# Kernel optimization log

Measured on AMD Instinct MI355X. Metric: run time of the kernel, lower is better.

Reference implementation:

```python
import jax, jax.numpy as jnp
import numpy as np

E = 8        # n_routed_experts
K = 2        # n_experts_per_token
H = 1024     # d_hidden
D = 512      # d_expert
NSH = 2      # n_shared_experts -> shared expert width = D*NSH


def setup_inputs() -> dict:
    key = jax.random.key(0)
    ks = jax.random.split(key, 8)
    s = 0.02
    x = jax.random.normal(ks[0], (4, 2048, H), jnp.float32)
    W_router = (jax.random.normal(ks[1], (H, E), jnp.float32) * s)
    Wg = (jax.random.normal(ks[2], (E, H, D), jnp.float32) * s)   # per-expert gate proj
    Wu = (jax.random.normal(ks[3], (E, H, D), jnp.float32) * s)   # per-expert up proj
    Wd = (jax.random.normal(ks[4], (E, D, H), jnp.float32) * s)   # per-expert down proj
    Ds = D * NSH
    Wsg = (jax.random.normal(ks[5], (H, Ds), jnp.float32) * s)
    Wsu = (jax.random.normal(ks[6], (H, Ds), jnp.float32) * s)
    Wsd = (jax.random.normal(ks[7], (Ds, H), jnp.float32) * s)
    return {"x": x, "W_router": W_router, "Wg": Wg, "Wu": Wu, "Wd": Wd,
            "Wsg": Wsg, "Wsu": Wsu, "Wsd": Wsd}


def reference(x, W_router, Wg, Wu, Wd, Wsg, Wsu, Wsd):
    B, S, Hd = x.shape
    T = B * S
    xf = x.reshape(T, Hd)

    # shared expert (SwiGLU)
    shared = (jax.nn.silu(xf @ Wsg) * (xf @ Wsu)) @ Wsd          # [T, H]

    # gating: softmax -> top-k -> renormalize
    logits = xf @ W_router                                        # [T, E]
    probs = jax.nn.softmax(logits, axis=-1)
    topk_scores, topk_idx = jax.lax.top_k(probs, K)               # [T, K]
    topk_scores = topk_scores / jnp.sum(topk_scores, axis=-1, keepdims=True)

    # combine weights: zero for unselected experts (topk indices are distinct,
    # so the original's first-match score selection equals a simple scatter)
    combine = jnp.zeros((T, E), x.dtype).at[jnp.arange(T)[:, None], topk_idx].set(topk_scores)

    # per-expert SwiGLU, computed densely and combined with sparse weights
    gate = jax.nn.silu(jnp.einsum('th,ehd->etd', xf, Wg))         # [E, T, D]
    up = jnp.einsum('th,ehd->etd', xf, Wu)                        # [E, T, D]
    expert_out = jnp.einsum('etd,edh->eth', gate * up, Wd)        # [E, T, H]
    routed = jnp.einsum('eth,te->th', expert_out, combine)        # [T, H]

    out = (routed + shared).reshape(B, S, Hd)

    # load-balancing aux loss: E * sum(mean_probs^2)
    probs_mean = jnp.mean(probs.reshape(B, S, E), axis=(0, 1))
    aux_loss = E * jnp.sum(probs_mean * probs_mean)
    return out, aux_loss
```

## Files before the change

### kernel.cpp

```cpp
#include <hip/hip_runtime.h>


typedef unsigned short u16;
typedef unsigned int   u32;
typedef short short8 __attribute__((ext_vector_type(8)));
typedef float f32x4  __attribute__((ext_vector_type(4)));

#define AS1 __attribute__((address_space(1)))
#define AS3 __attribute__((address_space(3)))

constexpr int T  = 8192;
constexpr int H  = 1024;
constexpr int E  = 8;
constexpr int D  = 512;
constexpr int DS = 1024;
constexpr int PAIR_CAP  = 17408;
constexpr int MT_ROUTED = 136;
constexpr int RB = 512;

constexpr int GU_ROUTED_BLKS = 8 * MT_ROUTED;
constexpr int GU_SHARED_BLKS = 16 * (T / 128);

__device__ __forceinline__ u16 f2bf(float f){
  u32 u = __builtin_bit_cast(u32, f);
  u += 0x7fffu + ((u >> 16) & 1u);
  return (u16)(u >> 16);
}
__device__ __forceinline__ float bf2f(u16 h){
  u32 u = ((u32)h) << 16;
  return __builtin_bit_cast(float, u);
}

__device__ __forceinline__ void gl_lds16(const u16* g, u16* l){
  __builtin_amdgcn_global_load_lds((const AS1 void*)g, (AS3 void*)l, 16, 0, 0);
}

__device__ __forceinline__ void wait_vmcnt8(){ __builtin_amdgcn_s_waitcnt(0x0f78); }
__device__ __forceinline__ void wait_vmcnt0(){ __builtin_amdgcn_s_waitcnt(0x0f70); }

__device__ __forceinline__ void bar_sync(){
  __builtin_amdgcn_fence(__ATOMIC_RELEASE, "workgroup", "local");
  __builtin_amdgcn_s_barrier();
  __builtin_amdgcn_fence(__ATOMIC_ACQUIRE, "workgroup", "local");
}

template<int ISS>
struct StagePtr { const u16* p[ISS]; };

template<int ROWS>
__device__ __forceinline__ void stage_init(StagePtr<ROWS/32>& sp,
    const u16* __restrict__ gbase, int ld, int rowbase,
    const int* __restrict__ gather, int wave, int lane){
  constexpr int ISS = ROWS / 32;
  int lr = lane >> 3, ch = lane & 7;
  int chs = (ch ^ lr) * 8;
#pragma unroll
  for (int j = 0; j < ISS; ++j){
    int idx = wave * ISS + j;
    int row = idx * 8 + lr;
    int grow = gather ? gather[rowbase + row] : (rowbase + row);
    sp.p[j] = gbase + (long)grow * ld + chs;
  }
}

template<int ROWS>
__device__ __forceinline__ void stage_issue(const StagePtr<ROWS/32>& sp, int k0,
                                            u16* lds, int wave, int lane){
  constexpr int ISS = ROWS / 32;
#pragma unroll
  for (int j = 0; j < ISS; ++j)
    gl_lds16(sp.p[j] + k0, lds + (wave * ISS + j) * 512);
}

__device__ __forceinline__ int swz_off(int c, int lane){
  return ((c ^ (lane & 7)) * 8);
}

__global__ void __launch_bounds__(256) router_kernel(
    const float* __restrict__ x, const float* __restrict__ Wr,
    u16* __restrict__ xb,
    int* __restrict__ topk_idx, float* __restrict__ topk_w,
    int* __restrict__ partial_hist, float* __restrict__ partial_probs)
{
  __shared__ int   hist_s[4][8];
  __shared__ float ps_s[4][8];
  int tid = threadIdx.x, lane = tid & 63, wv = tid >> 6;
  int   histl[8] = {0,0,0,0,0,0,0,0};
  float psl[8]   = {0.f,0.f,0.f,0.f,0.f,0.f,0.f,0.f};

  for (int it = 0; it < 4; ++it){
    int t = blockIdx.x * 16 + wv * 4 + it;
    const float4* xr = (const float4*)(x + (long)t * H);
    uint2* xbr = (uint2*)(xb + (long)t * H);
    float acc[8];
#pragma unroll
    for (int e = 0; e < 8; ++e) acc[e] = 0.f;
#pragma unroll
    for (int i = 0; i < 4; ++i){
      float4 xv = xr[i * 64 + lane];
      u32 lo = (u32)f2bf(xv.x) | ((u32)f2bf(xv.y) << 16);
      u32 hi = (u32)f2bf(xv.z) | ((u32)f2bf(xv.w) << 16);
      xbr[i * 64 + lane] = make_uint2(lo, hi);
      int h0 = i * 256 + lane * 4;
#pragma unroll
      for (int j = 0; j < 4; ++j){
        float xs = (j == 0) ? xv.x : (j == 1) ? xv.y : (j == 2) ? xv.z : xv.w;
        const float4* wr = (const float4*)(Wr + (long)(h0 + j) * E);
        float4 w0 = wr[0], w1 = wr[1];
        acc[0] += xs * w0.x; acc[1] += xs * w0.y; acc[2] += xs * w0.z; acc[3] += xs * w0.w;
        acc[4] += xs * w1.x; acc[5] += xs * w1.y; acc[6] += xs * w1.z; acc[7] += xs * w1.w;
      }
    }
#pragma unroll
    for (int off = 32; off >= 1; off >>= 1){
#pragma unroll
      for (int e = 0; e < 8; ++e) acc[e] += __shfl_xor(acc[e], off, 64);
    }
    if (lane == 0){
      float m = acc[0];
#pragma unroll
      for (int e = 1; e < 8; ++e) m = fmaxf(m, acc[e]);
      float p[8], s = 0.f;
#pragma unroll
      for (int e = 0; e < 8; ++e){ p[e] = __expf(acc[e] - m); s += p[e]; }
      float inv = 1.f / s;
#pragma unroll
      for (int e = 0; e < 8; ++e) psl[e] += p[e] * inv;
      int i1 = 0; float v1 = p[0];
#pragma unroll
      for (int e = 1; e < 8; ++e) if (p[e] > v1){ v1 = p[e]; i1 = e; }
      int i2 = -1; float v2 = -1.f;
#pragma unroll
      for (int e = 0; e < 8; ++e) if (e != i1 && p[e] > v2){ v2 = p[e]; i2 = e; }
      float rs = 1.f / (v1 + v2);
      topk_idx[2 * t] = i1; topk_idx[2 * t + 1] = i2;
      topk_w[2 * t] = v1 * rs; topk_w[2 * t + 1] = v2 * rs;
      histl[i1]++; histl[i2]++;
    }
  }
  if (lane == 0){
#pragma unroll
    for (int e = 0; e < 8; ++e){ hist_s[wv][e] = histl[e]; ps_s[wv][e] = psl[e]; }
  }
  __syncthreads();
  if (tid < 8){
    int hs = 0; float ps = 0.f;
#pragma unroll
    for (int w = 0; w < 4; ++w){ hs += hist_s[w][tid]; ps += ps_s[w][tid]; }
    partial_hist[blockIdx.x * 8 + tid]  = hs;
    partial_probs[blockIdx.x * 8 + tid] = ps;
  }
}

__global__ void __launch_bounds__(64) scan_kernel(
    const int* __restrict__ partial_hist, const float* __restrict__ partial_probs,
    int* __restrict__ block_offset, float* __restrict__ out_aux)
{
  __shared__ int   csum[8][8];
  __shared__ float cps[8][8];
  __shared__ int   cbase[8][8];
  __shared__ int   base_s[8];
  int tid = threadIdx.x, e = tid & 7, c = tid >> 3;
  int s = 0; float f = 0.f;
  for (int b = c * 64; b < c * 64 + 64; ++b){
    s += partial_hist[b * 8 + e]; f += partial_probs[b * 8 + e];
  }
  csum[c][e] = s; cps[c][e] = f;
  __syncthreads();
  if (tid < 8){
    int tot = 0;
    for (int cc = 0; cc < 8; ++cc){ cbase[cc][tid] = tot; tot += csum[cc][tid]; }
    csum[0][tid] = tot;
  }
  __syncthreads();
  if (tid == 0){
    int off = 0;
    for (int ee = 0; ee < 8; ++ee){ base_s[ee] = off; off += (csum[0][ee] + 127) & ~127; }
    float a = 0.f;
    for (int ee = 0; ee < 8; ++ee){
      float ps = 0.f;
      for (int cc = 0; cc < 8; ++cc) ps += cps[cc][ee];
      float m = ps * (1.f / (float)T);
      a += m * m;
    }
    out_aux[0] = (float)E * a;
  }
  __syncthreads();
  int run = base_s[e] + cbase[c][e];
  for (int b = c * 64; b < c * 64 + 64; ++b){
    block_offset[b * 8 + e] = run;
    run += partial_hist[b * 8 + e];
  }
}

__global__ void __launch_bounds__(64) scatter_kernel(
    const int* __restrict__ topk_idx, const float* __restrict__ topk_w,
    const int* __restrict__ block_offset,
    int* __restrict__ pair_token, int* __restrict__ pair_expert,
    float* __restrict__ pair_score, int* __restrict__ token_pos)
{
  int lane = threadIdx.x, b = blockIdx.x;
  if (lane >= 32) return;
  int idx = b * 32 + lane;
  int t = idx >> 1;
  int e = topk_idx[idx];
  float w = topk_w[idx];
  unsigned long long below = lane ? ((1ull << lane) - 1ull) : 0ull;
  int rank = 0, basee = 0;
#pragma unroll
  for (int ee = 0; ee < 8; ++ee){
    unsigned long long m = __ballot(e == ee);
    if (e == ee){ rank = __popcll(m & below); basee = block_offset[b * 8 + ee]; }
  }
  int pos = basee + rank;
  pair_token[pos] = t;
  pair_expert[pos] = e;
  pair_score[pos] = w;
  token_pos[idx] = pos;
}

__global__ void __launch_bounds__(256) transpose_all(
    const float* __restrict__ Wsg, u16* __restrict__ WsgT,
    const float* __restrict__ Wsu, u16* __restrict__ WsuT,
    const float* __restrict__ Wsd, u16* __restrict__ WsdT,
    const float* __restrict__ Wg,  u16* __restrict__ WgT,
    const float* __restrict__ Wu,  u16* __restrict__ WuT,
    const float* __restrict__ Wd,  u16* __restrict__ WdT)
{
  __shared__ float tile[32][33];
  int z = blockIdx.z;
  const float* src; u16* dst; int R, C;
  if (z < 3){
    R = 1024; C = 1024;
    src = (z == 0) ? Wsg : (z == 1) ? Wsu : Wsd;
    dst = (z == 0) ? WsgT : (z == 1) ? WsuT : WsdT;
  } else if (z < 19){
    R = 1024; C = 512;
    int p = z - 3;
    if (p < 8){ src = Wg + (long)p * R * C; dst = WgT + (long)p * R * C; }
    else      { src = Wu + (long)(p - 8) * R * C; dst = WuT + (long)(p - 8) * R * C; }
  } else {
    R = 512; C = 1024;
    int p = z - 19;
    src = Wd + (long)p * R * C; dst = WdT + (long)p * R * C;
  }
  int tx = threadIdx.x & 31, ty = threadIdx.x >> 5;
  int c = blockIdx.x * 32 + tx;
  int rb = blockIdx.y * 32;
  if (blockIdx.x * 32 >= C || rb >= R) return;
#pragma unroll
  for (int j = 0; j < 4; ++j)
    tile[ty + j * 8][tx] = src[(long)(rb + ty + j * 8) * C + c];
  __syncthreads();
#pragma unroll
  for (int j = 0; j < 4; ++j){
    int cc = blockIdx.x * 32 + ty + j * 8;
    dst[(long)cc * R + rb + tx] = f2bf(tile[tx][ty + j * 8]);
  }
}

__device__ __forceinline__ void gateup_body(
    const u16* __restrict__ A, const u16* __restrict__ Bg, const u16* __restrict__ Bu,
    u16* __restrict__ Hout, int N, int K,
    const int* __restrict__ gather, int mtile, int ntile,
    u16 (*As)[128 * 64], u16 (*Bgs)[64 * 64], u16 (*Bus)[64 * 64])
{
  int tid = threadIdx.x, lane = tid & 63, wave = tid >> 6;
  int wy = wave >> 1, wx = wave & 1;
  int m0 = mtile * 128, n0 = ntile * 64;
  int rl = lane & 15, q = lane >> 4;

  StagePtr<4> spA; StagePtr<2> spG; StagePtr<2> spU;
  stage_init<128>(spA, A, K, m0, gather, wave, lane);
  stage_init<64>(spG, Bg, K, n0, nullptr, wave, lane);
  stage_init<64>(spU, Bu, K, n0, nullptr, wave, lane);

  f32x4 accG[4][2], accU[4][2];
#pragma unroll
  for (int i = 0; i < 4; ++i)
#pragma unroll
    for (int j = 0; j < 2; ++j)
#pragma unroll
      for (int r = 0; r < 4; ++r){ accG[i][j][r] = 0.f; accU[i][j][r] = 0.f; }

  stage_issue<128>(spA, 0, As[0], wave, lane);
  stage_issue<64>(spG, 0, Bgs[0], wave, lane);
  stage_issue<64>(spU, 0, Bus[0], wave, lane);

  int NI = K / 64;
  for (int i = 0; i < NI; ++i){
    int cur = i & 1, nxt = cur ^ 1;
    if (i + 1 < NI){
      int kn = (i + 1) * 64;
      stage_issue<128>(spA, kn, As[nxt], wave, lane);
      stage_issue<64>(spG, kn, Bgs[nxt], wave, lane);
      stage_issue<64>(spU, kn, Bus[nxt], wave, lane);
      wait_vmcnt8();
    } else {
      wait_vmcnt0();
    }
    bar_sync();
#pragma unroll
    for (int ks = 0; ks < 2; ++ks){
      int off = swz_off(ks * 4 + q, lane);
      short8 a[4], g2[2], u2[2];
#pragma unroll
      for (int mt = 0; mt < 4; ++mt)
        a[mt] = *(const short8*)(As[cur] + (wy * 64 + mt * 16 + rl) * 64 + off);
#pragma unroll
      for (int nt = 0; nt < 2; ++nt){
        g2[nt] = *(const short8*)(Bgs[cur] + (wx * 32 + nt * 16 + rl) * 64 + off);
        u2[nt] = *(const short8*)(Bus[cur] + (wx * 32 + nt * 16 + rl) * 64 + off);
      }
#pragma unroll
      for (int mt = 0; mt < 4; ++mt)
#pragma unroll
        for (int nt = 0; nt < 2; ++nt){
          accG[mt][nt] = __builtin_amdgcn_mfma_f32_16x16x32_bf16(a[mt], g2[nt], accG[mt][nt], 0, 0, 0);
          accU[mt][nt] = __builtin_amdgcn_mfma_f32_16x16x32_bf16(a[mt], u2[nt], accU[mt][nt], 0, 0, 0);
        }
    }
    if (i + 1 < NI) bar_sync();
  }
  int row0 = m0 + wy * 64, col0 = n0 + wx * 32;
#pragma unroll
  for (int mt = 0; mt < 4; ++mt)
#pragma unroll
    for (int nt = 0; nt < 2; ++nt)
#pragma unroll
      for (int r = 0; r < 4; ++r){
        int row = row0 + mt * 16 + q * 4 + r;
        int col = col0 + nt * 16 + rl;
        float g = accG[mt][nt][r], u = accU[mt][nt][r];
        float h = g / (1.f + __expf(-g)) * u;
        Hout[(long)row * N + col] = f2bf(h);
      }
}

__global__ void __launch_bounds__(256) gateup_fused(
    const u16* __restrict__ xb,
    const u16* __restrict__ WgT, const u16* __restrict__ WuT, u16* __restrict__ hr,
    const u16* __restrict__ WsgT, const u16* __restrict__ WsuT, u16* __restrict__ hs,
    const int* __restrict__ pair_token, const int* __restrict__ pair_expert)
{
  __shared__ u16 As[2][128 * 64];
  __shared__ u16 Bgs[2][64 * 64];
  __shared__ u16 Bus[2][64 * 64];
  int fid = blockIdx.x;
  if (fid < GU_ROUTED_BLKS){
    int x8 = fid & 7, s = fid >> 3;
    int mtile = x8 + 8 * (s >> 3), ntile = s & 7;
    int e = pair_expert[mtile * 128];
    gateup_body(xb, WgT + (long)e * (D * H), WuT + (long)e * (D * H), hr,
                D, H, pair_token, mtile, ntile, As, Bgs, Bus);
  } else {
    int lid = fid - GU_ROUTED_BLKS;
    int x8 = lid & 7, s = lid >> 3;
    int mtile = x8 + 8 * (s >> 4), ntile = s & 15;
    gateup_body(xb, WsgT, WsuT, hs, DS, H, nullptr, mtile, ntile, As, Bgs, Bus);
  }
}

template<bool ROUTED>
__device__ __forceinline__ void down_body(
    const u16* __restrict__ A, const u16* __restrict__ B, int K,
    u16* __restrict__ rout, const float* __restrict__ pair_score,
    const int* __restrict__ token_pos, float* __restrict__ out,
    int mtile, int ntile, u16 (*As)[128 * 64], u16 (*Bs)[128 * 64])
{
  int tid = threadIdx.x, lane = tid & 63, wave = tid >> 6;
  int wy = wave >> 1, wx = wave & 1;
  int m0 = mtile * 128, n0 = ntile * 128;
  int rl = lane & 15, q = lane >> 4;

  StagePtr<4> spA, spB;
  stage_init<128>(spA, A, K, m0, nullptr, wave, lane);
  stage_init<128>(spB, B, K, n0, nullptr, wave, lane);

  f32x4 acc[4][4];
#pragma unroll
  for (int i = 0; i < 4; ++i)
#pragma unroll
    for (int j = 0; j < 4; ++j)
#pragma unroll
      for (int r = 0; r < 4; ++r) acc[i][j][r] = 0.f;

  stage_issue<128>(spA, 0, As[0], wave, lane);
  stage_issue<128>(spB, 0, Bs[0], wave, lane);

  int NI = K / 64;
  for (int i = 0; i < NI; ++i){
    int cur = i & 1, nxt = cur ^ 1;
    if (i + 1 < NI){
      int kn = (i + 1) * 64;
      stage_issue<128>(spA, kn, As[nxt], wave, lane);
      stage_issue<128>(spB, kn, Bs[nxt], wave, lane);
      wait_vmcnt8();
    } else {
      wait_vmcnt0();
    }
    bar_sync();
#pragma unroll
    for (int ks = 0; ks < 2; ++ks){
      int off = swz_off(ks * 4 + q, lane);
      short8 a[4], bv[4];
#pragma unroll
      for (int mt = 0; mt < 4; ++mt)
        a[mt] = *(const short8*)(As[cur] + (wy * 64 + mt * 16 + rl) * 64 + off);
#pragma unroll
      for (int nt = 0; nt < 4; ++nt)
        bv[nt] = *(const short8*)(Bs[cur] + (wx * 64 + nt * 16 + rl) * 64 + off);
#pragma unroll
      for (int mt = 0; mt < 4; ++mt)
#pragma unroll
        for (int nt = 0; nt < 4; ++nt)
          acc[mt][nt] = __builtin_amdgcn_mfma_f32_16x16x32_bf16(a[mt], bv[nt], acc[mt][nt], 0, 0, 0);
    }
    if (i + 1 < NI) bar_sync();
  }
#pragma unroll
  for (int mt = 0; mt < 4; ++mt)
#pragma unroll
    for (int r = 0; r < 4; ++r){
      int row = m0 + wy * 64 + mt * 16 + q * 4 + r;
      if (ROUTED){
        float s = pair_score[row];
        long rbase = (long)row * H;
#pragma unroll
        for (int nt = 0; nt < 4; ++nt){
          int col = n0 + wx * 64 + nt * 16 + rl;
          rout[rbase + col] = f2bf(s * acc[mt][nt][r]);
        }
      } else {
        int p0 = token_pos[2 * row], p1 = token_pos[2 * row + 1];
        long o = (long)row * H;
#pragma unroll
        for (int nt = 0; nt < 4; ++nt){
          int col = n0 + wx * 64 + nt * 16 + rl;
          out[o + col] = acc[mt][nt][r]
                       + bf2f(rout[(long)p0 * H + col])
                       + bf2f(rout[(long)p1 * H + col]);
        }
      }
    }
}

__global__ void __launch_bounds__(256) down_routed_kernel(
    const u16* __restrict__ A, const u16* __restrict__ B, u16* __restrict__ rout,
    const float* __restrict__ pair_score, const int* __restrict__ pexp)
{
  __shared__ u16 As[2][128 * 64];
  __shared__ u16 Bs[2][128 * 64];
  int fid = blockIdx.x;
  int x8 = fid & 7, s = fid >> 3;
  int mtile = x8 + 8 * (s >> 3), ntile = s & 7;
  int e = pexp[mtile * 128];
  down_body<true>(A, B + (long)e * (H * D), D, rout, pair_score, nullptr,
                  nullptr, mtile, ntile, As, Bs);
}

__global__ void __launch_bounds__(256) down_shared_kernel(
    const u16* __restrict__ A, const u16* __restrict__ B,
    const u16* __restrict__ rout, const int* __restrict__ token_pos,
    float* __restrict__ out)
{
  __shared__ u16 As[2][128 * 64];
  __shared__ u16 Bs[2][128 * 64];
  int fid = blockIdx.x;
  int x8 = fid & 7, s = fid >> 3;
  int mtile = x8 + 8 * (s >> 3), ntile = s & 7;
  down_body<false>(A, B, DS, const_cast<u16*>(rout), nullptr, token_pos, out,
                   mtile, ntile, As, Bs);
}

extern "C" void kernel_launch(void* const* d_in, const int* in_sizes, int n_in,
                              void* d_out, int out_size, void* d_ws, size_t ws_size,
                              hipStream_t stream)
{
  (void)in_sizes; (void)n_in; (void)out_size; (void)ws_size;
  const float* x   = (const float*)d_in[0];
  const float* Wr  = (const float*)d_in[1];
  const float* Wg  = (const float*)d_in[2];
  const float* Wu  = (const float*)d_in[3];
  const float* Wd  = (const float*)d_in[4];
  const float* Wsg = (const float*)d_in[5];
  const float* Wsu = (const float*)d_in[6];
  const float* Wsd = (const float*)d_in[7];
  float* out = (float*)d_out;

  char* ws = (char*)d_ws;
  size_t off = 0;
  auto alloc = [&](size_t bytes) -> void* {
    void* p = ws + off; off += (bytes + 255) & ~(size_t)255; return p;
  };
  u16* xb   = (u16*)alloc((size_t)T * H * 2);
  u16* WsgT = (u16*)alloc((size_t)DS * H * 2);
  u16* WsuT = (u16*)alloc((size_t)DS * H * 2);
  u16* WsdT = (u16*)alloc((size_t)H * DS * 2);
  u16* WgT  = (u16*)alloc((size_t)E * D * H * 2);
  u16* WuT  = (u16*)alloc((size_t)E * D * H * 2);
  u16* WdT  = (u16*)alloc((size_t)E * H * D * 2);
  u16* hs   = (u16*)alloc((size_t)T * DS * 2);
  u16* hr   = (u16*)alloc((size_t)PAIR_CAP * D * 2);
  u16* rout = (u16*)alloc((size_t)PAIR_CAP * H * 2);
  int*   topk_idx  = (int*)alloc((size_t)T * 2 * 4);
  float* topk_w    = (float*)alloc((size_t)T * 2 * 4);
  int*   token_pos = (int*)alloc((size_t)T * 2 * 4);
  int*   partial_hist  = (int*)alloc((size_t)RB * 8 * 4);
  float* partial_probs = (float*)alloc((size_t)RB * 8 * 4);
  int*   block_offset  = (int*)alloc((size_t)RB * 8 * 4);
  char* zbase = ws + off;
  int*   pair_token  = (int*)alloc((size_t)PAIR_CAP * 4);
  int*   pair_expert = (int*)alloc((size_t)PAIR_CAP * 4);
  float* pair_score  = (float*)alloc((size_t)PAIR_CAP * 4);
  size_t zbytes = (size_t)((ws + off) - zbase);

  hipMemsetAsync(zbase, 0, zbytes, stream);

  transpose_all<<<dim3(32, 32, 27), 256, 0, stream>>>(
      Wsg, WsgT, Wsu, WsuT, Wsd, WsdT, Wg, WgT, Wu, WuT, Wd, WdT);

  router_kernel<<<RB, 256, 0, stream>>>(x, Wr, xb, topk_idx, topk_w,
                                        partial_hist, partial_probs);
  scan_kernel<<<1, 64, 0, stream>>>(partial_hist, partial_probs, block_offset,
                                    out + (size_t)T * H);
  scatter_kernel<<<RB, 64, 0, stream>>>(topk_idx, topk_w, block_offset,
                                        pair_token, pair_expert, pair_score, token_pos);

  gateup_fused<<<GU_ROUTED_BLKS + GU_SHARED_BLKS, 256, 0, stream>>>(
      xb, WgT, WuT, hr, WsgT, WsuT, hs, pair_token, pair_expert);

  down_routed_kernel<<<8 * MT_ROUTED, 256, 0, stream>>>(
      hr, WdT, rout, pair_score, pair_expert);
  down_shared_kernel<<<8 * (T / 128), 256, 0, stream>>>(
      hs, WsdT, rout, token_pos, out);
}
```

Before: 327.3 us.

## Switch MoE GEMMs to 256x256 tiles with interleaved gate/up weights

Replaces the 128x64/128x128 GEMM tiles with a unified 256x256, 512-thread GEMM whose gate and up weights are interleaved in 16-row groups, so a single B operand produces both and the SwiGLU is applied in the epilogue. Expert segments are padded to 256 rows, and tiles past the actual pair count exit early using a count written by the scan kernel. The pipeline issues loads in halves between MFMA quarters, and the B tile is prefetched two steps ahead. Larger tiles raise operand reuse and cut global traffic, at the cost of more padding, fewer blocks and higher register pressure.

```diff
diff --git a/kernel.cpp b/kernel.cpp
--- a/kernel.cpp
+++ b/kernel.cpp
@@ -14,12 +14,14 @@
 constexpr int E  = 8;
 constexpr int D  = 512;
 constexpr int DS = 1024;
-constexpr int PAIR_CAP  = 17408;
-constexpr int MT_ROUTED = 136;
+constexpr int PAIR_CAP  = 18432;
+constexpr int MT_ROUTED = 72;
 constexpr int RB = 512;
 
-constexpr int GU_ROUTED_BLKS = 8 * MT_ROUTED;
-constexpr int GU_SHARED_BLKS = 16 * (T / 128);
+constexpr int GU_ROUTED_BLKS = 4 * MT_ROUTED;
+constexpr int GU_SHARED_BLKS = 8 * (T / 256);
+constexpr int DR_BLKS = 4 * MT_ROUTED;
+constexpr int DSH_BLKS = 4 * (T / 256);
 
 __device__ __forceinline__ u16 f2bf(float f){
   u32 u = __builtin_bit_cast(u32, f);
@@ -35,41 +37,13 @@
   __builtin_amdgcn_global_load_lds((const AS1 void*)g, (AS3 void*)l, 16, 0, 0);
 }
 
-__device__ __forceinline__ void wait_vmcnt8(){ __builtin_amdgcn_s_waitcnt(0x0f78); }
+__device__ __forceinline__ void wait_vmcnt4(){ __builtin_amdgcn_s_waitcnt(0x0f74); }
 __device__ __forceinline__ void wait_vmcnt0(){ __builtin_amdgcn_s_waitcnt(0x0f70); }
 
 __device__ __forceinline__ void bar_sync(){
   __builtin_amdgcn_fence(__ATOMIC_RELEASE, "workgroup", "local");
   __builtin_amdgcn_s_barrier();
   __builtin_amdgcn_fence(__ATOMIC_ACQUIRE, "workgroup", "local");
-}
-
-template<int ISS>
-struct StagePtr { const u16* p[ISS]; };
-
-template<int ROWS>
-__device__ __forceinline__ void stage_init(StagePtr<ROWS/32>& sp,
-    const u16* __restrict__ gbase, int ld, int rowbase,
-    const int* __restrict__ gather, int wave, int lane){
-  constexpr int ISS = ROWS / 32;
-  int lr = lane >> 3, ch = lane & 7;
-  int chs = (ch ^ lr) * 8;
-#pragma unroll
-  for (int j = 0; j < ISS; ++j){
-    int idx = wave * ISS + j;
-    int row = idx * 8 + lr;
-    int grow = gather ? gather[rowbase + row] : (rowbase + row);
-    sp.p[j] = gbase + (long)grow * ld + chs;
-  }
-}
-
-template<int ROWS>
-__device__ __forceinline__ void stage_issue(const StagePtr<ROWS/32>& sp, int k0,
-                                            u16* lds, int wave, int lane){
-  constexpr int ISS = ROWS / 32;
-#pragma unroll
-  for (int j = 0; j < ISS; ++j)
-    gl_lds16(sp.p[j] + k0, lds + (wave * ISS + j) * 512);
 }
 
 __device__ __forceinline__ int swz_off(int c, int lane){
@@ -154,7 +128,8 @@
 
 __global__ void __launch_bounds__(64) scan_kernel(
     const int* __restrict__ partial_hist, const float* __restrict__ partial_probs,
-    int* __restrict__ block_offset, float* __restrict__ out_aux)
+    int* __restrict__ block_offset, float* __restrict__ out_aux,
+    int* __restrict__ meta)
 {
   __shared__ int   csum[8][8];
   __shared__ float cps[8][8];
@@ -175,7 +150,8 @@
   __syncthreads();
   if (tid == 0){
     int off = 0;
-    for (int ee = 0; ee < 8; ++ee){ base_s[ee] = off; off += (csum[0][ee] + 127) & ~127; }
+    for (int ee = 0; ee < 8; ++ee){ base_s[ee] = off; off += (csum[0][ee] + 255) & ~255; }
+    meta[0] = off;
     float a = 0.f;
     for (int ee = 0; ee < 8; ++ee){
       float ps = 0.f;
@@ -220,29 +196,28 @@
 }
 
 __global__ void __launch_bounds__(256) transpose_all(
-    const float* __restrict__ Wsg, u16* __restrict__ WsgT,
-    const float* __restrict__ Wsu, u16* __restrict__ WsuT,
+    const float* __restrict__ Wsg, const float* __restrict__ Wsu, u16* __restrict__ WsguT,
     const float* __restrict__ Wsd, u16* __restrict__ WsdT,
-    const float* __restrict__ Wg,  u16* __restrict__ WgT,
-    const float* __restrict__ Wu,  u16* __restrict__ WuT,
+    const float* __restrict__ Wg,  const float* __restrict__ Wu, u16* __restrict__ WguT,
     const float* __restrict__ Wd,  u16* __restrict__ WdT)
 {
   __shared__ float tile[32][33];
   int z = blockIdx.z;
-  const float* src; u16* dst; int R, C;
+  const float* src; u16* dst; int R, C, itype;
   if (z < 3){
     R = 1024; C = 1024;
-    src = (z == 0) ? Wsg : (z == 1) ? Wsu : Wsd;
-    dst = (z == 0) ? WsgT : (z == 1) ? WsuT : WsdT;
+    if (z == 0){ src = Wsg; dst = WsguT; itype = 1; }
+    else if (z == 1){ src = Wsu; dst = WsguT; itype = 2; }
+    else { src = Wsd; dst = WsdT; itype = 0; }
   } else if (z < 19){
     R = 1024; C = 512;
     int p = z - 3;
-    if (p < 8){ src = Wg + (long)p * R * C; dst = WgT + (long)p * R * C; }
-    else      { src = Wu + (long)(p - 8) * R * C; dst = WuT + (long)(p - 8) * R * C; }
+    if (p < 8){ src = Wg + (long)p * R * C; dst = WguT + (long)p * (2 * D * H); itype = 1; }
+    else      { src = Wu + (long)(p - 8) * R * C; dst = WguT + (long)(p - 8) * (2 * D * H); itype = 2; }
   } else {
     R = 512; C = 1024;
     int p = z - 19;
-    src = Wd + (long)p * R * C; dst = WdT + (long)p * R * C;
+    src = Wd + (long)p * R * C; dst = WdT + (long)p * R * C; itype = 0;
   }
   int tx = threadIdx.x & 31, ty = threadIdx.x >> 5;
   int c = blockIdx.x * 32 + tx;
@@ -255,222 +230,221 @@
 #pragma unroll
   for (int j = 0; j < 4; ++j){
     int cc = blockIdx.x * 32 + ty + j * 8;
-    dst[(long)cc * R + rb + tx] = f2bf(tile[tx][ty + j * 8]);
-  }
-}
-
-__device__ __forceinline__ void gateup_body(
-    const u16* __restrict__ A, const u16* __restrict__ Bg, const u16* __restrict__ Bu,
-    u16* __restrict__ Hout, int N, int K,
-    const int* __restrict__ gather, int mtile, int ntile,
-    u16 (*As)[128 * 64], u16 (*Bgs)[64 * 64], u16 (*Bus)[64 * 64])
+    int dr = (itype == 0) ? cc : ((cc >> 4) * 32 + (cc & 15) + ((itype == 2) ? 16 : 0));
+    dst[(long)dr * R + rb + tx] = f2bf(tile[tx][ty + j * 8]);
+  }
+}
+
+struct HalfStage { const u16* p[2]; };
+
+__device__ __forceinline__ void half_init(HalfStage& hs, const u16* __restrict__ gbase,
+    int ld, int rowbase, const int* __restrict__ gather, int wave, int lane){
+  int lr = lane >> 3, ch = lane & 7;
+  int chs = (ch ^ lr) * 8;
+#pragma unroll
+  for (int j = 0; j < 2; ++j){
+    int row = (wave * 2 + j) * 8 + lr;
+    int grow = gather ? gather[rowbase + row] : (rowbase + row);
+    hs.p[j] = gbase + (long)grow * ld + chs;
+  }
+}
+
+__device__ __forceinline__ void half_issue(const HalfStage& hs, int k0,
+                                           u16* __restrict__ lds, int wave){
+#pragma unroll
+  for (int j = 0; j < 2; ++j)
+    gl_lds16(hs.p[j] + k0, lds + (wave * 2 + j) * 512);
+}
+
+template<int EPI>
+__device__ __forceinline__ void gemm256(
+    const u16* __restrict__ A, const u16* __restrict__ B, int K, int NT,
+    const int* __restrict__ gather, int m0, int n0,
+    u16* __restrict__ o_bf, int o_ld,
+    const float* __restrict__ pair_score,
+    const int* __restrict__ token_pos, const u16* __restrict__ rout,
+    float* __restrict__ out,
+    u16* __restrict__ As, u16* __restrict__ Bs)
 {
   int tid = threadIdx.x, lane = tid & 63, wave = tid >> 6;
-  int wy = wave >> 1, wx = wave & 1;
-  int m0 = mtile * 128, n0 = ntile * 64;
+  int wm = wave >> 2, wn = wave & 3;
   int rl = lane & 15, q = lane >> 4;
 
-  StagePtr<4> spA; StagePtr<2> spG; StagePtr<2> spU;
-  stage_init<128>(spA, A, K, m0, gather, wave, lane);
-  stage_init<64>(spG, Bg, K, n0, nullptr, wave, lane);
-  stage_init<64>(spU, Bu, K, n0, nullptr, wave, lane);
-
-  f32x4 accG[4][2], accU[4][2];
-#pragma unroll
-  for (int i = 0; i < 4; ++i)
-#pragma unroll
-    for (int j = 0; j < 2; ++j)
-#pragma unroll
-      for (int r = 0; r < 4; ++r){ accG[i][j][r] = 0.f; accU[i][j][r] = 0.f; }
-
-  stage_issue<128>(spA, 0, As[0], wave, lane);
-  stage_issue<64>(spG, 0, Bgs[0], wave, lane);
-  stage_issue<64>(spU, 0, Bus[0], wave, lane);
-
-  int NI = K / 64;
-  for (int i = 0; i < NI; ++i){
-    int cur = i & 1, nxt = cur ^ 1;
-    if (i + 1 < NI){
-      int kn = (i + 1) * 64;
-      stage_issue<128>(spA, kn, As[nxt], wave, lane);
-      stage_issue<64>(spG, kn, Bgs[nxt], wave, lane);
-      stage_issue<64>(spU, kn, Bus[nxt], wave, lane);
-      wait_vmcnt8();
-    } else {
-      wait_vmcnt0();
+  HalfStage a0, a1, b0, b1;
+  half_init(a0, A, K, m0,       gather, wave, lane);
+  half_init(a1, A, K, m0 + 128, gather, wave, lane);
+  half_init(b0, B, K, n0,       nullptr, wave, lane);
+  half_init(b1, B, K, n0 + 128, nullptr, wave, lane);
+
+  f32x4 acc[8][4];
+#pragma unroll
+  for (int i = 0; i < 8; ++i)
+#pragma unroll
+    for (int j = 0; j < 4; ++j)
+#pragma unroll
+      for (int r = 0; r < 4; ++r) acc[i][j][r] = 0.f;
+
+  half_issue(b0, 0, Bs + 0 * 8192, wave);
+  half_issue(b1, 0, Bs + 1 * 8192, wave);
+  half_issue(a0, 0, As + 0 * 8192, wave);
+  half_issue(a1, 0, As + 1 * 8192, wave);
+  if (NT > 1){
+    half_issue(b0, 64, Bs + 2 * 8192, wave);
+    half_issue(b1, 64, Bs + 3 * 8192, wave);
+    wait_vmcnt4();
+  } else {
+    wait_vmcnt0();
+  }
+  bar_sync();
+
+  int bhalf = wn >> 1, brow0 = (wn & 1) * 64;
+
+#pragma unroll 1
+  for (int t = 0; t < NT; ++t){
+    int buf = t & 1, nbuf = buf ^ 1;
+    const u16* Abase = As + (buf * 2 + wm) * 8192;
+    const u16* Bbase = Bs + (buf * 2 + bhalf) * 8192;
+    short8 bfr[2][4];
+#pragma unroll
+    for (int qd = 0; qd < 4; ++qd){
+      short8 afr[2][2];
+#pragma unroll
+      for (int ks = 0; ks < 2; ++ks){
+        int off = swz_off(ks * 4 + q, lane);
+#pragma unroll
+        for (int m = 0; m < 2; ++m)
+          afr[ks][m] = *(const short8*)(Abase + (qd * 32 + m * 16 + rl) * 64 + off);
+        if (qd == 0){
+#pragma unroll
+          for (int n = 0; n < 4; ++n)
+            bfr[ks][n] = *(const short8*)(Bbase + (brow0 + n * 16 + rl) * 64 + off);
+        }
+      }
+      if (qd == 0 && t + 1 < NT) half_issue(a0, (t + 1) * 64, As + (nbuf * 2 + 0) * 8192, wave);
+      if (qd == 1 && t + 1 < NT) half_issue(a1, (t + 1) * 64, As + (nbuf * 2 + 1) * 8192, wave);
+      if (qd == 2 && t + 2 < NT) half_issue(b0, (t + 2) * 64, Bs + (buf * 2 + 0) * 8192, wave);
+      if (qd == 3 && t + 2 < NT) half_issue(b1, (t + 2) * 64, Bs + (buf * 2 + 1) * 8192, wave);
+      bar_sync();
+      __builtin_amdgcn_s_setprio(1);
+#pragma unroll
+      for (int ks = 0; ks < 2; ++ks)
+#pragma unroll
+        for (int m = 0; m < 2; ++m)
+#pragma unroll
+          for (int n = 0; n < 4; ++n)
+            acc[qd * 2 + m][n] = __builtin_amdgcn_mfma_f32_16x16x32_bf16(
+                afr[ks][m], bfr[ks][n], acc[qd * 2 + m][n], 0, 0, 0);
+      __builtin_amdgcn_s_setprio(0);
+      if (qd == 3) wait_vmcnt4();
+      bar_sync();
     }
-    bar_sync();
-#pragma unroll
-    for (int ks = 0; ks < 2; ++ks){
-      int off = swz_off(ks * 4 + q, lane);
-      short8 a[4], g2[2], u2[2];
-#pragma unroll
-      for (int mt = 0; mt < 4; ++mt)
-        a[mt] = *(const short8*)(As[cur] + (wy * 64 + mt * 16 + rl) * 64 + off);
-#pragma unroll
-      for (int nt = 0; nt < 2; ++nt){
-        g2[nt] = *(const short8*)(Bgs[cur] + (wx * 32 + nt * 16 + rl) * 64 + off);
-        u2[nt] = *(const short8*)(Bus[cur] + (wx * 32 + nt * 16 + rl) * 64 + off);
-      }
-#pragma unroll
-      for (int mt = 0; mt < 4; ++mt)
-#pragma unroll
-        for (int nt = 0; nt < 2; ++nt){
-          accG[mt][nt] = __builtin_amdgcn_mfma_f32_16x16x32_bf16(a[mt], g2[nt], accG[mt][nt], 0, 0, 0);
-          accU[mt][nt] = __builtin_amdgcn_mfma_f32_16x16x32_bf16(a[mt], u2[nt], accU[mt][nt], 0, 0, 0);
+  }
+
+  int row0 = m0 + wm * 128;
+  if constexpr (EPI == 0){
+    int hcol0 = (n0 >> 1) + wn * 32;
+#pragma unroll
+    for (int mt = 0; mt < 8; ++mt)
+#pragma unroll
+      for (int ntp = 0; ntp < 2; ++ntp)
+#pragma unroll
+        for (int r = 0; r < 4; ++r){
+          int row = row0 + mt * 16 + q * 4 + r;
+          int col = hcol0 + ntp * 16 + rl;
+          float g = acc[mt][2 * ntp][r], u = acc[mt][2 * ntp + 1][r];
+          float h = g / (1.f + __expf(-g)) * u;
+          o_bf[(long)row * o_ld + col] = f2bf(h);
         }
-    }
-    if (i + 1 < NI) bar_sync();
-  }
-  int row0 = m0 + wy * 64, col0 = n0 + wx * 32;
-#pragma unroll
-  for (int mt = 0; mt < 4; ++mt)
-#pragma unroll
-    for (int nt = 0; nt < 2; ++nt)
+  } else if constexpr (EPI == 1){
+    int col0 = n0 + wn * 64;
+#pragma unroll
+    for (int mt = 0; mt < 8; ++mt)
 #pragma unroll
       for (int r = 0; r < 4; ++r){
         int row = row0 + mt * 16 + q * 4 + r;
-        int col = col0 + nt * 16 + rl;
-        float g = accG[mt][nt][r], u = accU[mt][nt][r];
-        float h = g / (1.f + __expf(-g)) * u;
-        Hout[(long)row * N + col] = f2bf(h);
-      }
-}
-
-__global__ void __launch_bounds__(256) gateup_fused(
-    const u16* __restrict__ xb,
-    const u16* __restrict__ WgT, const u16* __restrict__ WuT, u16* __restrict__ hr,
-    const u16* __restrict__ WsgT, const u16* __restrict__ WsuT, u16* __restrict__ hs,
-    const int* __restrict__ pair_token, const int* __restrict__ pair_expert)
-{
-  __shared__ u16 As[2][128 * 64];
-  __shared__ u16 Bgs[2][64 * 64];
-  __shared__ u16 Bus[2][64 * 64];
-  int fid = blockIdx.x;
-  if (fid < GU_ROUTED_BLKS){
-    int x8 = fid & 7, s = fid >> 3;
-    int mtile = x8 + 8 * (s >> 3), ntile = s & 7;
-    int e = pair_expert[mtile * 128];
-    gateup_body(xb, WgT + (long)e * (D * H), WuT + (long)e * (D * H), hr,
-                D, H, pair_token, mtile, ntile, As, Bgs, Bus);
-  } else {
-    int lid = fid - GU_ROUTED_BLKS;
-    int x8 = lid & 7, s = lid >> 3;
-    int mtile = x8 + 8 * (s >> 4), ntile = s & 15;
-    gateup_body(xb, WsgT, WsuT, hs, DS, H, nullptr, mtile, ntile, As, Bgs, Bus);
-  }
-}
-
-template<bool ROUTED>
-__device__ __forceinline__ void down_body(
-    const u16* __restrict__ A, const u16* __restrict__ B, int K,
-    u16* __restrict__ rout, const float* __restrict__ pair_score,
-    const int* __restrict__ token_pos, float* __restrict__ out,
-    int mtile, int ntile, u16 (*As)[128 * 64], u16 (*Bs)[128 * 64])
-{
-  int tid = threadIdx.x, lane = tid & 63, wave = tid >> 6;
-  int wy = wave >> 1, wx = wave & 1;
-  int m0 = mtile * 128, n0 = ntile * 128;
-  int rl = lane & 15, q = lane >> 4;
-
-  StagePtr<4> spA, spB;
-  stage_init<128>(spA, A, K, m0, nullptr, wave, lane);
-  stage_init<128>(spB, B, K, n0, nullptr, wave, lane);
-
-  f32x4 acc[4][4];
-#pragma unroll
-  for (int i = 0; i < 4; ++i)
-#pragma unroll
-    for (int j = 0; j < 4; ++j)
-#pragma unroll
-      for (int r = 0; r < 4; ++r) acc[i][j][r] = 0.f;
-
-  stage_issue<128>(spA, 0, As[0], wave, lane);
-  stage_issue<128>(spB, 0, Bs[0], wave, lane);
-
-  int NI = K / 64;
-  for (int i = 0; i < NI; ++i){
-    int cur = i & 1, nxt = cur ^ 1;
-    if (i + 1 < NI){
-      int kn = (i + 1) * 64;
-      stage_issue<128>(spA, kn, As[nxt], wave, lane);
-      stage_issue<128>(spB, kn, Bs[nxt], wave, lane);
-      wait_vmcnt8();
-    } else {
-      wait_vmcnt0();
-    }
-    bar_sync();
-#pragma unroll
-    for (int ks = 0; ks < 2; ++ks){
-      int off = swz_off(ks * 4 + q, lane);
-      short8 a[4], bv[4];
-#pragma unroll
-      for (int mt = 0; mt < 4; ++mt)
-        a[mt] = *(const short8*)(As[cur] + (wy * 64 + mt * 16 + rl) * 64 + off);
-#pragma unroll
-      for (int nt = 0; nt < 4; ++nt)
-        bv[nt] = *(const short8*)(Bs[cur] + (wx * 64 + nt * 16 + rl) * 64 + off);
-#pragma unroll
-      for (int mt = 0; mt < 4; ++mt)
-#pragma unroll
-        for (int nt = 0; nt < 4; ++nt)
-          acc[mt][nt] = __builtin_amdgcn_mfma_f32_16x16x32_bf16(a[mt], bv[nt], acc[mt][nt], 0, 0, 0);
-    }
-    if (i + 1 < NI) bar_sync();
-  }
-#pragma unroll
-  for (int mt = 0; mt < 4; ++mt)
-#pragma unroll
-    for (int r = 0; r < 4; ++r){
-      int row = m0 + wy * 64 + mt * 16 + q * 4 + r;
-      if (ROUTED){
         float s = pair_score[row];
         long rbase = (long)row * H;
 #pragma unroll
-        for (int nt = 0; nt < 4; ++nt){
-          int col = n0 + wx * 64 + nt * 16 + rl;
-          rout[rbase + col] = f2bf(s * acc[mt][nt][r]);
+        for (int n = 0; n < 4; ++n){
+          int col = col0 + n * 16 + rl;
+          o_bf[rbase + col] = f2bf(s * acc[mt][n][r]);
         }
-      } else {
+      }
+  } else {
+    int col0 = n0 + wn * 64;
+#pragma unroll
+    for (int mt = 0; mt < 8; ++mt)
+#pragma unroll
+      for (int r = 0; r < 4; ++r){
+        int row = row0 + mt * 16 + q * 4 + r;
         int p0 = token_pos[2 * row], p1 = token_pos[2 * row + 1];
         long o = (long)row * H;
 #pragma unroll
-        for (int nt = 0; nt < 4; ++nt){
-          int col = n0 + wx * 64 + nt * 16 + rl;
-          out[o + col] = acc[mt][nt][r]
+        for (int n = 0; n < 4; ++n){
+          int col = col0 + n * 16 + rl;
+          out[o + col] = acc[mt][n][r]
                        + bf2f(rout[(long)p0 * H + col])
                        + bf2f(rout[(long)p1 * H + col]);
         }
       }
-    }
-}
-
-__global__ void __launch_bounds__(256) down_routed_kernel(
-    const u16* __restrict__ A, const u16* __restrict__ B, u16* __restrict__ rout,
-    const float* __restrict__ pair_score, const int* __restrict__ pexp)
-{
-  __shared__ u16 As[2][128 * 64];
-  __shared__ u16 Bs[2][128 * 64];
+  }
+}
+
+__global__ void __launch_bounds__(512, 2) gateup_fused(
+    const u16* __restrict__ xb, const u16* __restrict__ WguT, u16* __restrict__ hr,
+    const u16* __restrict__ WsguT, u16* __restrict__ hs,
+    const int* __restrict__ pair_token, const int* __restrict__ pair_expert,
+    const int* __restrict__ meta)
+{
+  __shared__ u16 As[4 * 8192];
+  __shared__ u16 Bs[4 * 8192];
+  int fid = blockIdx.x;
+  if (fid < GU_ROUTED_BLKS){
+    int x8 = fid & 7, s = fid >> 3;
+    int mtile = x8 + 8 * (s >> 2), ntile = s & 3;
+    int m0 = mtile * 256;
+    if (m0 >= meta[0]) return;
+    int e = pair_expert[m0];
+    gemm256<0>(xb, WguT + (long)e * (2 * D * H), H, H / 64, pair_token,
+               m0, ntile * 256, hr, D, nullptr, nullptr, nullptr, nullptr, As, Bs);
+  } else {
+    int lid = fid - GU_ROUTED_BLKS;
+    int x8 = lid & 7, s = lid >> 3;
+    int mtile = x8 + 8 * (s >> 3), ntile = s & 7;
+    gemm256<0>(xb, WsguT, H, H / 64, nullptr,
+               mtile * 256, ntile * 256, hs, DS, nullptr, nullptr, nullptr, nullptr, As, Bs);
+  }
+}
+
+__global__ void __launch_bounds__(512, 2) down_routed_kernel(
+    const u16* __restrict__ hr, const u16* __restrict__ WdT, u16* __restrict__ rout,
+    const float* __restrict__ pair_score, const int* __restrict__ pair_expert,
+    const int* __restrict__ meta)
+{
+  __shared__ u16 As[4 * 8192];
+  __shared__ u16 Bs[4 * 8192];
   int fid = blockIdx.x;
   int x8 = fid & 7, s = fid >> 3;
-  int mtile = x8 + 8 * (s >> 3), ntile = s & 7;
-  int e = pexp[mtile * 128];
-  down_body<true>(A, B + (long)e * (H * D), D, rout, pair_score, nullptr,
-                  nullptr, mtile, ntile, As, Bs);
-}
-
-__global__ void __launch_bounds__(256) down_shared_kernel(
-    const u16* __restrict__ A, const u16* __restrict__ B,
+  int mtile = x8 + 8 * (s >> 2), ntile = s & 3;
+  int m0 = mtile * 256;
+  if (m0 >= meta[0]) return;
+  int e = pair_expert[m0];
+  gemm256<1>(hr, WdT + (long)e * (H * D), D, D / 64, nullptr,
+             m0, ntile * 256, rout, H, pair_score, nullptr, nullptr, nullptr, As, Bs);
+}
+
+__global__ void __launch_bounds__(512, 2) down_shared_kernel(
+    const u16* __restrict__ hs, const u16* __restrict__ WsdT,
     const u16* __restrict__ rout, const int* __restrict__ token_pos,
     float* __restrict__ out)
 {
-  __shared__ u16 As[2][128 * 64];
-  __shared__ u16 Bs[2][128 * 64];
+  __shared__ u16 As[4 * 8192];
+  __shared__ u16 Bs[4 * 8192];
   int fid = blockIdx.x;
   int x8 = fid & 7, s = fid >> 3;
-  int mtile = x8 + 8 * (s >> 3), ntile = s & 7;
-  down_body<false>(A, B, DS, const_cast<u16*>(rout), nullptr, token_pos, out,
-                   mtile, ntile, As, Bs);
+  int mtile = x8 + 8 * (s >> 2), ntile = s & 3;
+  gemm256<2>(hs, WsdT, DS, DS / 64, nullptr,
+             mtile * 256, ntile * 256, nullptr, 0, nullptr, token_pos, rout, out, As, Bs);
 }
 
 extern "C" void kernel_launch(void* const* d_in, const int* in_sizes, int n_in,
@@ -493,22 +467,21 @@
   auto alloc = [&](size_t bytes) -> void* {
     void* p = ws + off; off += (bytes + 255) & ~(size_t)255; return p;
   };
-  u16* xb   = (u16*)alloc((size_t)T * H * 2);
-  u16* WsgT = (u16*)alloc((size_t)DS * H * 2);
-  u16* WsuT = (u16*)alloc((size_t)DS * H * 2);
-  u16* WsdT = (u16*)alloc((size_t)H * DS * 2);
-  u16* WgT  = (u16*)alloc((size_t)E * D * H * 2);
-  u16* WuT  = (u16*)alloc((size_t)E * D * H * 2);
-  u16* WdT  = (u16*)alloc((size_t)E * H * D * 2);
-  u16* hs   = (u16*)alloc((size_t)T * DS * 2);
-  u16* hr   = (u16*)alloc((size_t)PAIR_CAP * D * 2);
-  u16* rout = (u16*)alloc((size_t)PAIR_CAP * H * 2);
+  u16* xb    = (u16*)alloc((size_t)T * H * 2);
+  u16* WsguT = (u16*)alloc((size_t)2 * DS * H * 2);
+  u16* WsdT  = (u16*)alloc((size_t)H * DS * 2);
+  u16* WguT  = (u16*)alloc((size_t)E * 2 * D * H * 2);
+  u16* WdT   = (u16*)alloc((size_t)E * H * D * 2);
+  u16* hs    = (u16*)alloc((size_t)T * DS * 2);
+  u16* hr    = (u16*)alloc((size_t)PAIR_CAP * D * 2);
+  u16* rout  = (u16*)alloc((size_t)PAIR_CAP * H * 2);
   int*   topk_idx  = (int*)alloc((size_t)T * 2 * 4);
   float* topk_w    = (float*)alloc((size_t)T * 2 * 4);
   int*   token_pos = (int*)alloc((size_t)T * 2 * 4);
   int*   partial_hist  = (int*)alloc((size_t)RB * 8 * 4);
   float* partial_probs = (float*)alloc((size_t)RB * 8 * 4);
   int*   block_offset  = (int*)alloc((size_t)RB * 8 * 4);
+  int*   meta          = (int*)alloc(256);
   char* zbase = ws + off;
   int*   pair_token  = (int*)alloc((size_t)PAIR_CAP * 4);
   int*   pair_expert = (int*)alloc((size_t)PAIR_CAP * 4);
@@ -518,20 +491,20 @@
   hipMemsetAsync(zbase, 0, zbytes, stream);
 
   transpose_all<<<dim3(32, 32, 27), 256, 0, stream>>>(
-      Wsg, WsgT, Wsu, WsuT, Wsd, WsdT, Wg, WgT, Wu, WuT, Wd, WdT);
+      Wsg, Wsu, WsguT, Wsd, WsdT, Wg, Wu, WguT, Wd, WdT);
 
   router_kernel<<<RB, 256, 0, stream>>>(x, Wr, xb, topk_idx, topk_w,
                                         partial_hist, partial_probs);
   scan_kernel<<<1, 64, 0, stream>>>(partial_hist, partial_probs, block_offset,
-                                    out + (size_t)T * H);
+                                    out + (size_t)T * H, meta);
   scatter_kernel<<<RB, 64, 0, stream>>>(topk_idx, topk_w, block_offset,
                                         pair_token, pair_expert, pair_score, token_pos);
 
-  gateup_fused<<<GU_ROUTED_BLKS + GU_SHARED_BLKS, 256, 0, stream>>>(
-      xb, WgT, WuT, hr, WsgT, WsuT, hs, pair_token, pair_expert);
-
-  down_routed_kernel<<<8 * MT_ROUTED, 256, 0, stream>>>(
-      hr, WdT, rout, pair_score, pair_expert);
-  down_shared_kernel<<<8 * (T / 128), 256, 0, stream>>>(
+  gateup_fused<<<GU_ROUTED_BLKS + GU_SHARED_BLKS, 512, 0, stream>>>(
+      xb, WguT, hr, WsguT, hs, pair_token, pair_expert, meta);
+
+  down_routed_kernel<<<DR_BLKS, 512, 0, stream>>>(
+      hr, WdT, rout, pair_score, pair_expert, meta);
+  down_shared_kernel<<<DSH_BLKS, 512, 0, stream>>>(
       hs, WsdT, rout, token_pos, out);
 }
```

Measured after the change: 421.2 us. 28.7% more time.
